# Kernel tuning notes

Measured on AMD Instinct MI355X. Metric: run time of the kernel, lower is better.

The kernel has to match this reference:

```python
import jax, jax.numpy as jnp
import numpy as np

N_NODES = 100000
N_EDGES = 1600000
D_IN = 16
D_HID = 32   # 2 * out_channels
D_OUT = 16


def gcn_conv(h, src, dst, W, b, num_nodes):
    """PyG-style GCNConv: x' = D^{-1/2} (A+I) D^{-1/2} (x W) + b.
    src/dst already include self-loops."""
    h = h @ W                                   # [N, F_out] linear transform first
    deg = jnp.zeros((num_nodes,), h.dtype).at[dst].add(1.0)
    dinv = jax.lax.rsqrt(jnp.maximum(deg, 1.0))  # deg >= 1 due to self-loops
    norm = dinv[src] * dinv[dst]                # [E+N]
    msg = h[src] * norm[:, None]                # edge gather (memory-bound)
    out = jax.ops.segment_sum(msg, dst, num_segments=num_nodes)
    return out + b


def setup_inputs() -> dict:
    key = jax.random.key(0)
    k1, k2, k3, k4 = jax.random.split(key, 4)
    x = jnp.arange(N_NODES, dtype=jnp.int32)
    edge_index = jax.random.randint(k1, (2, N_EDGES), 0, N_NODES, dtype=jnp.int32)
    emb = jax.random.normal(k2, (N_NODES, D_IN), dtype=jnp.float32)
    W1 = jax.random.normal(k3, (D_IN, D_HID), dtype=jnp.float32) * (1.0 / np.sqrt(D_IN))
    b1 = jnp.zeros((D_HID,), jnp.float32)
    W2 = jax.random.normal(k4, (D_HID, D_OUT), dtype=jnp.float32) * (1.0 / np.sqrt(D_HID))
    b2 = jnp.zeros((D_OUT,), jnp.float32)
    return {"x": x, "edge_index": edge_index, "emb": emb,
            "W1": W1, "b1": b1, "W2": W2, "b2": b2}


def reference(x, edge_index, emb, W1, b1, W2, b2):
    num_nodes = emb.shape[0]
    # add self-loops once; reused by both conv layers
    loops = jnp.arange(num_nodes, dtype=edge_index.dtype)
    src = jnp.concatenate([edge_index[0], loops])
    dst = jnp.concatenate([edge_index[1], loops])

    h = emb[x]                                  # embedding lookup
    h = jax.nn.relu(gcn_conv(h, src, dst, W1, b1, num_nodes))
    # dropout is identity in eval mode (reference baseline)
    out = gcn_conv(h, src, dst, W2, b2, num_nodes)
    return out
```

## Files before the change

### kernel.cpp

```cpp
#include <hip/hip_runtime.h>


#define BS   256
#define NBLK 256
#define BINSHIFT 8
#define BIN  256
#define MAXBINS 512
#define BINCAP 4608

union H2 { int i; _Float16 h[2]; };

__global__ void k_hist(const int* __restrict__ dst, int E, int NBINS,
                       int* __restrict__ histG) {
    __shared__ int h[MAXBINS];
    int t = threadIdx.x;
    for (int i = t; i < NBINS; i += BS) h[i] = 0;
    __syncthreads();
    int E4 = E >> 2;
    const int4* d4 = (const int4*)dst;
    for (int i = blockIdx.x * BS + t; i < E4; i += NBLK * BS) {
        int4 d = d4[i];
        atomicAdd(&h[d.x >> BINSHIFT], 1);
        atomicAdd(&h[d.y >> BINSHIFT], 1);
        atomicAdd(&h[d.z >> BINSHIFT], 1);
        atomicAdd(&h[d.w >> BINSHIFT], 1);
    }
    if (blockIdx.x == 0 && t < (E & 3))
        atomicAdd(&h[dst[(E4 << 2) + t] >> BINSHIFT], 1);
    __syncthreads();
    for (int i = t; i < NBINS; i += BS) histG[i * NBLK + blockIdx.x] = h[i];
}

__global__ void k_scanA(const int* __restrict__ in, int L,
                        int* __restrict__ partial, int* __restrict__ bsum) {
    __shared__ int s[BS];
    int t = threadIdx.x;
    int i = blockIdx.x * BS + t;
    int v = (i < L) ? in[i] : 0;
    s[t] = v;
    __syncthreads();
    for (int off = 1; off < BS; off <<= 1) {
        int add = (t >= off) ? s[t - off] : 0;
        __syncthreads();
        s[t] += add;
        __syncthreads();
    }
    if (i < L) partial[i] = s[t] - v;
    if (t == BS - 1) bsum[blockIdx.x] = s[BS - 1];
}

__global__ void k_scanB(const int* __restrict__ bsum, int nB, int* __restrict__ boff) {
    __shared__ int s[BS];
    int t = threadIdx.x;
    int PER = (nB + BS - 1) / BS;
    int loc[8];
    int base = t * PER;
    int sum = 0;
    for (int j = 0; j < PER && j < 8; j++) {
        int idx = base + j;
        int v = (idx < nB) ? bsum[idx] : 0;
        loc[j] = sum;
        sum += v;
    }
    s[t] = sum;
    __syncthreads();
    for (int off = 1; off < BS; off <<= 1) {
        int add = (t >= off) ? s[t - off] : 0;
        __syncthreads();
        s[t] += add;
        __syncthreads();
    }
    int ex = s[t] - sum;
    for (int j = 0; j < PER && j < 8; j++) {
        int idx = base + j;
        if (idx < nB) boff[idx] = ex + loc[j];
    }
}

__global__ void k_binscatter(const int* __restrict__ src, const int* __restrict__ dst,
                             int E, int NBINS, const int* __restrict__ partial,
                             const int* __restrict__ boff, int* __restrict__ packed) {
    __shared__ int cur[MAXBINS];
    int t = threadIdx.x;
    for (int i = t; i < NBINS; i += BS)
        cur[i] = partial[i * NBLK + blockIdx.x] + boff[i];
    __syncthreads();
    int E4 = E >> 2;
    const int4* s4 = (const int4*)src;
    const int4* d4 = (const int4*)dst;
    for (int i = blockIdx.x * BS + t; i < E4; i += NBLK * BS) {
        int4 s = s4[i];
        int4 d = d4[i];
        int p0 = atomicAdd(&cur[d.x >> BINSHIFT], 1);
        packed[p0] = s.x | ((d.x & (BIN - 1)) << 18);
        int p1 = atomicAdd(&cur[d.y >> BINSHIFT], 1);
        packed[p1] = s.y | ((d.y & (BIN - 1)) << 18);
        int p2 = atomicAdd(&cur[d.z >> BINSHIFT], 1);
        packed[p2] = s.z | ((d.z & (BIN - 1)) << 18);
        int p3 = atomicAdd(&cur[d.w >> BINSHIFT], 1);
        packed[p3] = s.w | ((d.w & (BIN - 1)) << 18);
    }
    if (blockIdx.x == 0 && t < (E & 3)) {
        int e = (E4 << 2) + t;
        int d = dst[e];
        int p = atomicAdd(&cur[d >> BINSHIFT], 1);
        packed[p] = src[e] | ((d & (BIN - 1)) << 18);
    }
}

__global__ void k_binsort(const int* __restrict__ packed,
                          const int* __restrict__ partial, const int* __restrict__ boff,
                          int NBINS, int N, int E,
                          const int* __restrict__ x, const float* __restrict__ emb,
                          const float* __restrict__ W1,
                          int* __restrict__ row_start, float* __restrict__ dinv,
                          int* __restrict__ col, _Float16* __restrict__ sig1) {
    __shared__ int buf[BINCAP];
    __shared__ int ldeg[BIN];
    __shared__ int lrs[BIN];
    __shared__ int cur[BIN];
    __shared__ float sW[512];
    int b = blockIdx.x;
    int t = threadIdx.x;
    int node0 = b << BINSHIFT;
    int e0 = partial[b * NBLK] + boff[b];
    int e1 = (b + 1 < NBINS) ? (partial[(b + 1) * NBLK] + boff[b + 1]) : E;
    int cnt = e1 - e0;
    bool fits = (cnt <= BINCAP);
    if (b == 0 && t == 0) row_start[N] = E;
    sW[t] = W1[t];
    sW[t + 256] = W1[t + 256];
    ldeg[t] = 0;
    if (fits)
        for (int i = t; i < cnt; i += BS) buf[i] = packed[e0 + i];
    __syncthreads();
    for (int i = t; i < cnt; i += BS) {
        int v = fits ? buf[i] : packed[e0 + i];
        atomicAdd(&ldeg[((unsigned)v >> 18) & (BIN - 1)], 1);
    }
    __syncthreads();
    lrs[t] = ldeg[t];
    __syncthreads();
    for (int off = 1; off < BIN; off <<= 1) {
        int add = (t >= off) ? lrs[t - off] : 0;
        __syncthreads();
        lrs[t] += add;
        __syncthreads();
    }
    int myDeg = ldeg[t];
    int ex = lrs[t] - myDeg;
    cur[t] = ex;
    int n = node0 + t;
    float di = rsqrtf((float)(myDeg + 1));
    if (n < N) {
        row_start[n] = e0 + ex;
        dinv[n] = di;
    }
    __syncthreads();
    for (int i = t; i < cnt; i += BS) {
        int v = fits ? buf[i] : packed[e0 + i];
        int pos = atomicAdd(&cur[((unsigned)v >> 18) & (BIN - 1)], 1);
        col[e0 + pos] = v & 0x3FFFF;
    }
    if (n < N) {
        const float4* er = (const float4*)(emb + (size_t)x[n] * 16);
        float4 ra = er[0], rb = er[1], rc = er[2], rd = er[3];
        float ev[16] = {ra.x, ra.y, ra.z, ra.w, rb.x, rb.y, rb.z, rb.w,
                        rc.x, rc.y, rc.z, rc.w, rd.x, rd.y, rd.z, rd.w};
        int4* s1o = (int4*)sig1;
        #pragma unroll
        for (int cq = 0; cq < 4; cq++) {
            H2 pk[4];
            #pragma unroll
            for (int dw = 0; dw < 4; dw++) {
                int c = cq * 8 + dw * 2;
                float acc0 = 0.f, acc1 = 0.f;
                #pragma unroll
                for (int k = 0; k < 16; k++) {
                    acc0 += ev[k] * sW[k * 32 + c];
                    acc1 += ev[k] * sW[k * 32 + c + 1];
                }
                pk[dw].h[0] = (_Float16)(acc0 * di);
                pk[dw].h[1] = (_Float16)(acc1 * di);
            }
            int4 pv;
            pv.x = pk[0].i; pv.y = pk[1].i; pv.z = pk[2].i; pv.w = pk[3].i;
            s1o[(size_t)n * 4 + cq] = pv;
        }
    }
}

__global__ __launch_bounds__(BS) void k_agg1mm2(
    const _Float16* __restrict__ sig1, const int* __restrict__ row_start,
    const float* __restrict__ dinv, const int* __restrict__ col,
    const float* __restrict__ b1, const float* __restrict__ W2,
    int N, _Float16* __restrict__ sig2) {
    __shared__ float hbuf[4][4][36];
    int t = threadIdx.x;
    int lane = t & 63;
    int wid = t >> 6;
    int g  = lane >> 4;
    int cd = lane & 15;
    int n = blockIdx.x * 16 + wid * 4 + g;
    int nld = (n < N) ? n : N - 1;
    int rs = row_start[nld];
    int re = row_start[nld + 1];
    int dn = (n < N) ? (re - rs) : 0;
    int dnm1 = (dn > 0) ? dn - 1 : 0;
    int dm = dn;
    dm = max(dm, __shfl_xor(dm, 16));
    dm = max(dm, __shfl_xor(dm, 32));
    float w2c[32];
    #pragma unroll
    for (int k = 0; k < 32; k++) w2c[k] = W2[k * 16 + cd];
    const int* s1i = (const int*)sig1;
    float a0 = 0.f, a1 = 0.f;
    int iters = (dm + 3) >> 2;
    int slot = cd & 3;
    int bidx = lane & 48;
    for (int it = 0; it < iters; it++) {
        int e = it << 2;
        int idx = e + slot; if (idx > dnm1) idx = dnm1;
        int colv = col[rs + idx];
        int s0 = __shfl(colv, bidx + 0);
        int s1 = __shfl(colv, bidx + 1);
        int s2 = __shfl(colv, bidx + 2);
        int s3 = __shfl(colv, bidx + 3);
        int u0 = s1i[s0 * 16 + cd];
        int u1 = s1i[s1 * 16 + cd];
        int u2 = s1i[s2 * 16 + cd];
        int u3 = s1i[s3 * 16 + cd];
        u0 = (e + 0 < dn) ? u0 : 0;
        u1 = (e + 1 < dn) ? u1 : 0;
        u2 = (e + 2 < dn) ? u2 : 0;
        u3 = (e + 3 < dn) ? u3 : 0;
        H2 p0, p1, p2, p3;
        p0.i = u0; p1.i = u1; p2.i = u2; p3.i = u3;
        a0 += ((float)p0.h[0] + (float)p1.h[0]) + ((float)p2.h[0] + (float)p3.h[0]);
        a1 += ((float)p0.h[1] + (float)p1.h[1]) + ((float)p2.h[1] + (float)p3.h[1]);
    }
    {
        H2 p; p.i = s1i[nld * 16 + cd];
        a0 += (float)p.h[0];
        a1 += (float)p.h[1];
    }
    float di = dinv[nld];
    float2 b = ((const float2*)b1)[cd];
    float h0 = fmaxf(a0 * di + b.x, 0.f);
    float h1 = fmaxf(a1 * di + b.y, 0.f);
    float* hb = hbuf[wid][g];
    *(float2*)&hb[2 * cd] = make_float2(h0, h1);
    float a = 0.f;
    #pragma unroll
    for (int k = 0; k < 32; k += 4) {
        float4 hv = *(const float4*)&hb[k];
        a = fmaf(hv.x, w2c[k],     a);
        a = fmaf(hv.y, w2c[k + 1], a);
        a = fmaf(hv.z, w2c[k + 2], a);
        a = fmaf(hv.w, w2c[k + 3], a);
    }
    if (n < N) sig2[(size_t)n * 16 + cd] = (_Float16)(a * di);
}

__global__ __launch_bounds__(BS) void k_agg2(
    const _Float16* __restrict__ sig2, const int* __restrict__ row_start,
    const float* __restrict__ dinv, const int* __restrict__ col,
    const float* __restrict__ b2, int N, float* __restrict__ out) {
    int t = threadIdx.x;
    int lane = t & 63;
    int g  = lane >> 4;
    int e2 = (lane >> 3) & 1;
    int cd = lane & 7;
    int n = blockIdx.x * 16 + (t >> 6) * 4 + g;
    int nld = (n < N) ? n : N - 1;
    int rs = row_start[nld];
    int re = row_start[nld + 1];
    int dn = (n < N) ? (re - rs) : 0;
    int dnm1 = (dn > 0) ? dn - 1 : 0;
    int dm = dn;
    dm = max(dm, __shfl_xor(dm, 16));
    dm = max(dm, __shfl_xor(dm, 32));
    const int* s2i = (const int*)sig2;
    float a0 = 0.f, a1 = 0.f;
    int iters = (dm + 7) >> 3;
    int slot = lane & 7;
    int bidx = lane & 48;
    for (int it = 0; it < iters; it++) {
        int e = it << 3;
        int idx = e + slot; if (idx > dnm1) idx = dnm1;
        int colv = col[rs + idx];
        #pragma unroll
        for (int j = 0; j < 4; j++) {
            int sl = 2 * j + e2;
            int sv = __shfl(colv, bidx + sl);
            int u = s2i[sv * 8 + cd];
            u = (e + sl < dn) ? u : 0;
            H2 p; p.i = u;
            a0 += (float)p.h[0];
            a1 += (float)p.h[1];
        }
    }
    a0 += __shfl_xor(a0, 8);
    a1 += __shfl_xor(a1, 8);
    {
        H2 p; p.i = s2i[nld * 8 + cd];
        a0 += (float)p.h[0];
        a1 += (float)p.h[1];
    }
    if (n < N && e2 == 0) {
        float di = dinv[nld];
        float2 b = ((const float2*)b2)[cd];
        float2 o;
        o.x = a0 * di + b.x;
        o.y = a1 * di + b.y;
        ((float2*)out)[(size_t)n * 8 + cd] = o;
    }
}

extern "C" void kernel_launch(void* const* d_in, const int* in_sizes, int n_in,
                              void* d_out, int out_size, void* d_ws, size_t ws_size,
                              hipStream_t stream) {
    const int*   x   = (const int*)d_in[0];
    const int*   ei  = (const int*)d_in[1];
    const float* emb = (const float*)d_in[2];
    const float* W1  = (const float*)d_in[3];
    const float* b1  = (const float*)d_in[4];
    const float* W2  = (const float*)d_in[5];
    const float* b2  = (const float*)d_in[6];
    float* out = (float*)d_out;

    const int N = in_sizes[0];
    const int E = in_sizes[1] / 2;
    const int* srcp = ei;
    const int* dstp = ei + E;
    const int NBINS = (N + BIN - 1) >> BINSHIFT;
    const int L = NBINS * NBLK;
    const int nB2 = (L + BS - 1) / BS;

    auto al = [](size_t b) { return (b + 255) & ~size_t(255); };
    char* w = (char*)d_ws;
    auto carve = [&](size_t bytes) {
        void* p = (void*)w;
        w += al(bytes);
        return p;
    };
    int*   row_start = (int*)carve((size_t)(N + 1) * 4);
    float* dinv      = (float*)carve((size_t)N * 4);
    int*   col       = (int*)carve((size_t)(E + 256) * 4);
    int*   histG     = (int*)carve((size_t)L * 4);
    int*   partial   = (int*)carve((size_t)L * 4);
    int*   bsum      = (int*)carve((size_t)nB2 * 4);
    int*   boff      = (int*)carve((size_t)nB2 * 4);
    int*   packed    = (int*)carve((size_t)E * 4);
    _Float16* sig1   = (_Float16*)carve((size_t)N * 32 * 2);
    _Float16* sig2   = (_Float16*)carve((size_t)N * 16 * 2);
    (void)ws_size; (void)n_in; (void)out_size;

    int gL = (L + BS - 1) / BS;
    k_hist<<<NBLK, BS, 0, stream>>>(dstp, E, NBINS, histG);
    k_scanA<<<gL, BS, 0, stream>>>(histG, L, partial, bsum);
    k_scanB<<<1, BS, 0, stream>>>(bsum, nB2, boff);
    k_binscatter<<<NBLK, BS, 0, stream>>>(srcp, dstp, E, NBINS, partial, boff, packed);
    k_binsort<<<NBINS, BS, 0, stream>>>(packed, partial, boff, NBINS, N, E,
                                        x, emb, W1, row_start, dinv, col, sig1);

    int gA = (N + 15) / 16;
    k_agg1mm2<<<gA, BS, 0, stream>>>(sig1, row_start, dinv, col, b1, W2, N, sig2);
    k_agg2<<<gA, BS, 0, stream>>>(sig2, row_start, dinv, col, b2, N, out);
}
```

Measured before the change: 159.4 us.

## Fuse CSR build into one cooperative kernel and prefetch column indices

```diff
diff --git a/kernel.cpp b/kernel.cpp
--- a/kernel.cpp
+++ b/kernel.cpp
@@ -1,8 +1,11 @@
 #include <hip/hip_runtime.h>
+#include <hip/hip_cooperative_groups.h>
+
+namespace cg = cooperative_groups;
 
 
 #define BS   256
-#define NBLK 256
+#define GRID 256
 #define BINSHIFT 8
 #define BIN  256
 #define MAXBINS 512
@@ -10,56 +13,52 @@
 
 union H2 { int i; _Float16 h[2]; };
 
-__global__ void k_hist(const int* __restrict__ dst, int E, int NBINS,
-                       int* __restrict__ histG) {
+__global__ void __launch_bounds__(BS) k_build(
+    const int* __restrict__ src, const int* __restrict__ dst, int E, int NBINS,
+    int N, const int* __restrict__ x, const float* __restrict__ emb,
+    const float* __restrict__ W1, int* __restrict__ histG, int* __restrict__ bsum,
+    int* __restrict__ boff, int* __restrict__ row_start, float* __restrict__ dinv,
+    int* __restrict__ col, _Float16* __restrict__ sig1, int* __restrict__ packed) {
+    cg::grid_group grid = cg::this_grid();
     __shared__ int h[MAXBINS];
+    __shared__ int s[BS];
+    __shared__ int buf[BINCAP];
+    __shared__ int ldeg[BIN];
+    __shared__ int lrs[BIN];
+    __shared__ int cur[BIN];
+    __shared__ float sW[512];
     int t = threadIdx.x;
+    int b = blockIdx.x;
+    int E4 = E >> 2;
+    const int4* d4 = (const int4*)dst;
+
     for (int i = t; i < NBINS; i += BS) h[i] = 0;
     __syncthreads();
-    int E4 = E >> 2;
-    const int4* d4 = (const int4*)dst;
-    for (int i = blockIdx.x * BS + t; i < E4; i += NBLK * BS) {
+    for (int i = b * BS + t; i < E4; i += GRID * BS) {
         int4 d = d4[i];
         atomicAdd(&h[d.x >> BINSHIFT], 1);
         atomicAdd(&h[d.y >> BINSHIFT], 1);
         atomicAdd(&h[d.z >> BINSHIFT], 1);
         atomicAdd(&h[d.w >> BINSHIFT], 1);
     }
-    if (blockIdx.x == 0 && t < (E & 3))
+    if (b == 0 && t < (E & 3))
         atomicAdd(&h[dst[(E4 << 2) + t] >> BINSHIFT], 1);
     __syncthreads();
-    for (int i = t; i < NBINS; i += BS) histG[i * NBLK + blockIdx.x] = h[i];
-}
-
-__global__ void k_scanA(const int* __restrict__ in, int L,
-                        int* __restrict__ partial, int* __restrict__ bsum) {
-    __shared__ int s[BS];
-    int t = threadIdx.x;
-    int i = blockIdx.x * BS + t;
-    int v = (i < L) ? in[i] : 0;
-    s[t] = v;
-    __syncthreads();
-    for (int off = 1; off < BS; off <<= 1) {
-        int add = (t >= off) ? s[t - off] : 0;
-        __syncthreads();
-        s[t] += add;
-        __syncthreads();
-    }
-    if (i < L) partial[i] = s[t] - v;
-    if (t == BS - 1) bsum[blockIdx.x] = s[BS - 1];
-}
-
-__global__ void k_scanB(const int* __restrict__ bsum, int nB, int* __restrict__ boff) {
-    __shared__ int s[BS];
-    int t = threadIdx.x;
-    int PER = (nB + BS - 1) / BS;
-    int loc[8];
-    int base = t * PER;
+    for (int i = t; i < NBINS; i += BS) histG[i * GRID + b] = h[i];
+    if (b == 0 && t == 0) row_start[N] = E;
+    grid.sync();
+
+    int L = NBINS * GRID;
+    int tid = b * BS + t;
+    const int T = GRID * BS;
+    int PER = (L + T - 1) / T;
+    int vloc[4];
+    int base0 = tid * PER;
     int sum = 0;
-    for (int j = 0; j < PER && j < 8; j++) {
-        int idx = base + j;
-        int v = (idx < nB) ? bsum[idx] : 0;
-        loc[j] = sum;
+    for (int j = 0; j < PER && j < 4; j++) {
+        int idx = base0 + j;
+        int v = (idx < L) ? histG[idx] : 0;
+        vloc[j] = v;
         sum += v;
     }
     s[t] = sum;
@@ -70,122 +69,123 @@
         s[t] += add;
         __syncthreads();
     }
-    int ex = s[t] - sum;
-    for (int j = 0; j < PER && j < 8; j++) {
-        int idx = base + j;
-        if (idx < nB) boff[idx] = ex + loc[j];
-    }
-}
-
-__global__ void k_binscatter(const int* __restrict__ src, const int* __restrict__ dst,
-                             int E, int NBINS, const int* __restrict__ partial,
-                             const int* __restrict__ boff, int* __restrict__ packed) {
-    __shared__ int cur[MAXBINS];
-    int t = threadIdx.x;
-    for (int i = t; i < NBINS; i += BS)
-        cur[i] = partial[i * NBLK + blockIdx.x] + boff[i];
+    int exi = s[t] - sum;
+    if (t == BS - 1) bsum[b] = s[BS - 1];
+    grid.sync();
+
+    if (b == 0) {
+        int v = bsum[t];
+        s[t] = v;
+        __syncthreads();
+        for (int off = 1; off < BS; off <<= 1) {
+            int add = (t >= off) ? s[t - off] : 0;
+            __syncthreads();
+            s[t] += add;
+            __syncthreads();
+        }
+        boff[t] = s[t] - v;
+    }
+    grid.sync();
+
+    {
+        int base = boff[b] + exi;
+        for (int j = 0; j < PER && j < 4; j++) {
+            int idx = base0 + j;
+            if (idx < L) histG[idx] = base;
+            base += vloc[j];
+        }
+    }
+    grid.sync();
+
+    for (int i = t; i < NBINS; i += BS) h[i] = histG[i * GRID + b];
     __syncthreads();
-    int E4 = E >> 2;
     const int4* s4 = (const int4*)src;
-    const int4* d4 = (const int4*)dst;
-    for (int i = blockIdx.x * BS + t; i < E4; i += NBLK * BS) {
-        int4 s = s4[i];
-        int4 d = d4[i];
-        int p0 = atomicAdd(&cur[d.x >> BINSHIFT], 1);
-        packed[p0] = s.x | ((d.x & (BIN - 1)) << 18);
-        int p1 = atomicAdd(&cur[d.y >> BINSHIFT], 1);
-        packed[p1] = s.y | ((d.y & (BIN - 1)) << 18);
-        int p2 = atomicAdd(&cur[d.z >> BINSHIFT], 1);
-        packed[p2] = s.z | ((d.z & (BIN - 1)) << 18);
-        int p3 = atomicAdd(&cur[d.w >> BINSHIFT], 1);
-        packed[p3] = s.w | ((d.w & (BIN - 1)) << 18);
-    }
-    if (blockIdx.x == 0 && t < (E & 3)) {
+    for (int i = b * BS + t; i < E4; i += GRID * BS) {
+        int4 sv = s4[i];
+        int4 dv = d4[i];
+        int p0 = atomicAdd(&h[dv.x >> BINSHIFT], 1);
+        packed[p0] = sv.x | ((dv.x & (BIN - 1)) << 18);
+        int p1 = atomicAdd(&h[dv.y >> BINSHIFT], 1);
+        packed[p1] = sv.y | ((dv.y & (BIN - 1)) << 18);
+        int p2 = atomicAdd(&h[dv.z >> BINSHIFT], 1);
+        packed[p2] = sv.z | ((dv.z & (BIN - 1)) << 18);
+        int p3 = atomicAdd(&h[dv.w >> BINSHIFT], 1);
+        packed[p3] = sv.w | ((dv.w & (BIN - 1)) << 18);
+    }
+    if (b == 0 && t < (E & 3)) {
         int e = (E4 << 2) + t;
         int d = dst[e];
-        int p = atomicAdd(&cur[d >> BINSHIFT], 1);
+        int p = atomicAdd(&h[d >> BINSHIFT], 1);
         packed[p] = src[e] | ((d & (BIN - 1)) << 18);
     }
-}
-
-__global__ void k_binsort(const int* __restrict__ packed,
-                          const int* __restrict__ partial, const int* __restrict__ boff,
-                          int NBINS, int N, int E,
-                          const int* __restrict__ x, const float* __restrict__ emb,
-                          const float* __restrict__ W1,
-                          int* __restrict__ row_start, float* __restrict__ dinv,
-                          int* __restrict__ col, _Float16* __restrict__ sig1) {
-    __shared__ int buf[BINCAP];
-    __shared__ int ldeg[BIN];
-    __shared__ int lrs[BIN];
-    __shared__ int cur[BIN];
-    __shared__ float sW[512];
-    int b = blockIdx.x;
-    int t = threadIdx.x;
-    int node0 = b << BINSHIFT;
-    int e0 = partial[b * NBLK] + boff[b];
-    int e1 = (b + 1 < NBINS) ? (partial[(b + 1) * NBLK] + boff[b + 1]) : E;
-    int cnt = e1 - e0;
-    bool fits = (cnt <= BINCAP);
-    if (b == 0 && t == 0) row_start[N] = E;
+    grid.sync();
+
     sW[t] = W1[t];
     sW[t + 256] = W1[t + 256];
-    ldeg[t] = 0;
-    if (fits)
-        for (int i = t; i < cnt; i += BS) buf[i] = packed[e0 + i];
-    __syncthreads();
-    for (int i = t; i < cnt; i += BS) {
-        int v = fits ? buf[i] : packed[e0 + i];
-        atomicAdd(&ldeg[((unsigned)v >> 18) & (BIN - 1)], 1);
-    }
-    __syncthreads();
-    lrs[t] = ldeg[t];
-    __syncthreads();
-    for (int off = 1; off < BIN; off <<= 1) {
-        int add = (t >= off) ? lrs[t - off] : 0;
-        __syncthreads();
-        lrs[t] += add;
-        __syncthreads();
-    }
-    int myDeg = ldeg[t];
-    int ex = lrs[t] - myDeg;
-    cur[t] = ex;
-    int n = node0 + t;
-    float di = rsqrtf((float)(myDeg + 1));
-    if (n < N) {
-        row_start[n] = e0 + ex;
-        dinv[n] = di;
-    }
-    __syncthreads();
-    for (int i = t; i < cnt; i += BS) {
-        int v = fits ? buf[i] : packed[e0 + i];
-        int pos = atomicAdd(&cur[((unsigned)v >> 18) & (BIN - 1)], 1);
-        col[e0 + pos] = v & 0x3FFFF;
-    }
-    if (n < N) {
-        const float4* er = (const float4*)(emb + (size_t)x[n] * 16);
-        float4 ra = er[0], rb = er[1], rc = er[2], rd = er[3];
-        float ev[16] = {ra.x, ra.y, ra.z, ra.w, rb.x, rb.y, rb.z, rb.w,
-                        rc.x, rc.y, rc.z, rc.w, rd.x, rd.y, rd.z, rd.w};
-        int4* s1o = (int4*)sig1;
-        #pragma unroll
-        for (int cq = 0; cq < 4; cq++) {
-            H2 pk[4];
+    for (int bin = b; bin < NBINS; bin += GRID) {
+        __syncthreads();
+        int node0 = bin << BINSHIFT;
+        int e0 = histG[bin * GRID];
+        int e1 = (bin + 1 < NBINS) ? histG[(bin + 1) * GRID] : E;
+        int cnt = e1 - e0;
+        bool fits = (cnt <= BINCAP);
+        ldeg[t] = 0;
+        if (fits)
+            for (int i = t; i < cnt; i += BS) buf[i] = packed[e0 + i];
+        __syncthreads();
+        for (int i = t; i < cnt; i += BS) {
+            int v = fits ? buf[i] : packed[e0 + i];
+            atomicAdd(&ldeg[((unsigned)v >> 18) & (BIN - 1)], 1);
+        }
+        __syncthreads();
+        lrs[t] = ldeg[t];
+        __syncthreads();
+        for (int off = 1; off < BIN; off <<= 1) {
+            int add = (t >= off) ? lrs[t - off] : 0;
+            __syncthreads();
+            lrs[t] += add;
+            __syncthreads();
+        }
+        int myDeg = ldeg[t];
+        int ex = lrs[t] - myDeg;
+        cur[t] = ex;
+        int n = node0 + t;
+        float di = rsqrtf((float)(myDeg + 1));
+        if (n < N) {
+            row_start[n] = e0 + ex;
+            dinv[n] = di;
+        }
+        __syncthreads();
+        for (int i = t; i < cnt; i += BS) {
+            int v = fits ? buf[i] : packed[e0 + i];
+            int pos = atomicAdd(&cur[((unsigned)v >> 18) & (BIN - 1)], 1);
+            col[e0 + pos] = v & 0x3FFFF;
+        }
+        if (n < N) {
+            const float4* er = (const float4*)(emb + (size_t)x[n] * 16);
+            float4 ra = er[0], rb = er[1], rc = er[2], rd = er[3];
+            float ev[16] = {ra.x, ra.y, ra.z, ra.w, rb.x, rb.y, rb.z, rb.w,
+                            rc.x, rc.y, rc.z, rc.w, rd.x, rd.y, rd.z, rd.w};
+            int4* s1o = (int4*)sig1;
             #pragma unroll
-            for (int dw = 0; dw < 4; dw++) {
-                int c = cq * 8 + dw * 2;
-                float acc0 = 0.f, acc1 = 0.f;
+            for (int cq = 0; cq < 4; cq++) {
+                H2 pk[4];
                 #pragma unroll
-                for (int k = 0; k < 16; k++) {
-                    acc0 += ev[k] * sW[k * 32 + c];
-                    acc1 += ev[k] * sW[k * 32 + c + 1];
+                for (int dw = 0; dw < 4; dw++) {
+                    int c = cq * 8 + dw * 2;
+                    float acc0 = 0.f, acc1 = 0.f;
+                    #pragma unroll
+                    for (int k = 0; k < 16; k++) {
+                        acc0 += ev[k] * sW[k * 32 + c];
+                        acc1 += ev[k] * sW[k * 32 + c + 1];
+                    }
+                    pk[dw].h[0] = (_Float16)(acc0 * di);
+                    pk[dw].h[1] = (_Float16)(acc1 * di);
                 }
-                pk[dw].h[0] = (_Float16)(acc0 * di);
-                pk[dw].h[1] = (_Float16)(acc1 * di);
+                int4 pv;
+                pv.x = pk[0].i; pv.y = pk[1].i; pv.z = pk[2].i; pv.w = pk[3].i;
+                s1o[(size_t)n * 4 + cq] = pv;
             }
-            int4 pv;
-            pv.x = pk[0].i; pv.y = pk[1].i; pv.z = pk[2].i; pv.w = pk[3].i;
-            s1o[(size_t)n * 4 + cq] = pv;
         }
     }
 }
@@ -218,10 +218,18 @@
     int iters = (dm + 3) >> 2;
     int slot = cd & 3;
     int bidx = lane & 48;
+    int colv = 0;
+    if (iters > 0) {
+        int idx = slot; if (idx > dnm1) idx = dnm1;
+        colv = col[rs + idx];
+    }
     for (int it = 0; it < iters; it++) {
         int e = it << 2;
-        int idx = e + slot; if (idx > dnm1) idx = dnm1;
-        int colv = col[rs + idx];
+        int coln = 0;
+        if (it + 1 < iters) {
+            int idx = e + 4 + slot; if (idx > dnm1) idx = dnm1;
+            coln = col[rs + idx];
+        }
         int s0 = __shfl(colv, bidx + 0);
         int s1 = __shfl(colv, bidx + 1);
         int s2 = __shfl(colv, bidx + 2);
@@ -238,6 +246,7 @@
         p0.i = u0; p1.i = u1; p2.i = u2; p3.i = u3;
         a0 += ((float)p0.h[0] + (float)p1.h[0]) + ((float)p2.h[0] + (float)p3.h[0]);
         a1 += ((float)p0.h[1] + (float)p1.h[1]) + ((float)p2.h[1] + (float)p3.h[1]);
+        colv = coln;
     }
     {
         H2 p; p.i = s1i[nld * 16 + cd];
@@ -285,10 +294,18 @@
     int iters = (dm + 7) >> 3;
     int slot = lane & 7;
     int bidx = lane & 48;
+    int colv = 0;
+    if (iters > 0) {
+        int idx = slot; if (idx > dnm1) idx = dnm1;
+        colv = col[rs + idx];
+    }
     for (int it = 0; it < iters; it++) {
         int e = it << 3;
-        int idx = e + slot; if (idx > dnm1) idx = dnm1;
-        int colv = col[rs + idx];
+        int coln = 0;
+        if (it + 1 < iters) {
+            int idx = e + 8 + slot; if (idx > dnm1) idx = dnm1;
+            coln = col[rs + idx];
+        }
         #pragma unroll
         for (int j = 0; j < 4; j++) {
             int sl = 2 * j + e2;
@@ -299,6 +316,7 @@
             a0 += (float)p.h[0];
             a1 += (float)p.h[1];
         }
+        colv = coln;
     }
     a0 += __shfl_xor(a0, 8);
     a1 += __shfl_xor(a1, 8);
@@ -334,8 +352,7 @@
     const int* srcp = ei;
     const int* dstp = ei + E;
     const int NBINS = (N + BIN - 1) >> BINSHIFT;
-    const int L = NBINS * NBLK;
-    const int nB2 = (L + BS - 1) / BS;
+    const int L = NBINS * GRID;
 
     auto al = [](size_t b) { return (b + 255) & ~size_t(255); };
     char* w = (char*)d_ws;
@@ -348,21 +365,24 @@
     float* dinv      = (float*)carve((size_t)N * 4);
     int*   col       = (int*)carve((size_t)(E + 256) * 4);
     int*   histG     = (int*)carve((size_t)L * 4);
-    int*   partial   = (int*)carve((size_t)L * 4);
-    int*   bsum      = (int*)carve((size_t)nB2 * 4);
-    int*   boff      = (int*)carve((size_t)nB2 * 4);
+    int*   bsum      = (int*)carve((size_t)GRID * 4);
+    int*   boff      = (int*)carve((size_t)GRID * 4);
     int*   packed    = (int*)carve((size_t)E * 4);
     _Float16* sig1   = (_Float16*)carve((size_t)N * 32 * 2);
     _Float16* sig2   = (_Float16*)carve((size_t)N * 16 * 2);
     (void)ws_size; (void)n_in; (void)out_size;
 
-    int gL = (L + BS - 1) / BS;
-    k_hist<<<NBLK, BS, 0, stream>>>(dstp, E, NBINS, histG);
-    k_scanA<<<gL, BS, 0, stream>>>(histG, L, partial, bsum);
-    k_scanB<<<1, BS, 0, stream>>>(bsum, nB2, boff);
-    k_binscatter<<<NBLK, BS, 0, stream>>>(srcp, dstp, E, NBINS, partial, boff, packed);
-    k_binsort<<<NBINS, BS, 0, stream>>>(packed, partial, boff, NBINS, N, E,
-                                        x, emb, W1, row_start, dinv, col, sig1);
+    {
+        int En = E, NBn = NBINS, Nn = N;
+        void* args[] = {
+            (void*)&srcp, (void*)&dstp, (void*)&En, (void*)&NBn, (void*)&Nn,
+            (void*)&x, (void*)&emb, (void*)&W1, (void*)&histG, (void*)&bsum,
+            (void*)&boff, (void*)&row_start, (void*)&dinv, (void*)&col,
+            (void*)&sig1, (void*)&packed
+        };
+        hipLaunchCooperativeKernel((void*)k_build, dim3(GRID), dim3(BS),
+                                   args, 0, stream);
+    }
 
     int gA = (N + 15) / 16;
     k_agg1mm2<<<gA, BS, 0, stream>>>(sig1, row_start, dinv, col, b1, W2, N, sig2);
```

After: 320.6 us. 101% more time.
